# Optimization experiments

Measured on AMD Instinct MI355X. Metric: run time of the kernel, lower is better.

Reference implementation:

```python
import jax, jax.numpy as jnp
import numpy as np


def setup_inputs() -> dict:
    key = jax.random.key(0)
    k1, k2, k3 = jax.random.split(key, 3)
    B, F, D = 1024, 784, 512
    x = jax.random.normal(k1, (B, F), dtype=jnp.float32)
    # keras 'uniform' initializer ~ U(-0.05, 0.05)
    Wmin = jax.random.uniform(k2, (D, F), dtype=jnp.float32, minval=-0.05, maxval=0.05)
    Wmax = jax.random.uniform(k3, (D, F), dtype=jnp.float32, minval=-0.05, maxval=0.05)
    return {"x": x, "Wmin": Wmin, "Wmax": Wmax}


def reference(x, Wmin, Wmax):
    # x: [B, F]; Wmin, Wmax: [D, F]
    # L1[b,d] = min_f (x[b,f] - Wmin[d,f]); L2[b,d] = min_f (Wmax[d,f] - x[b,f])
    L1 = jnp.min(x[:, None, :] - Wmin[None, :, :], axis=2)  # [B, D]
    L2 = jnp.min(Wmax[None, :, :] - x[:, None, :], axis=2)  # [B, D]
    # activation is None (linear) in this config
    return jnp.minimum(L1, L2)  # [B, D]
```

## Files before the change

kernel.cpp:

```cpp
#include <hip/hip_runtime.h>


constexpr int F_DIM = 784;
constexpr int BK = 8;
constexpr int NCHUNK = F_DIM / BK;
constexpr int BM = 32;
constexpr int BN = 128;
constexpr int LSTR = BK + 4;
constexpr int ZSPLIT = 16;

typedef float f4v __attribute__((ext_vector_type(4)));
typedef float f2v __attribute__((ext_vector_type(2)));

__global__ __launch_bounds__(64, 3)
void dendral_main(const float* __restrict__ x,
                  const float* __restrict__ wmin,
                  const float* __restrict__ wmax,
                  float* __restrict__ dst,
                  int D, long long sliceN, int zsplit) {
  __shared__ float lx[BM * LSTR];
  __shared__ float lwn[BN * LSTR];
  __shared__ float lwx[BN * LSTR];

  const int l  = threadIdx.x;
  const int tx = l & 15;
  const int ty = l >> 4;
  const int b0 = blockIdx.x * BM;
  const int d0 = blockIdx.y * BN;
  const int z  = blockIdx.z;
  const int c0 = (z * NCHUNK) / zsplit;
  const int c1 = ((z + 1) * NCHUNK) / zsplit;

  const int sr = l >> 1;
  const int sc = (l & 1) << 2;
  const float* xg = x + (size_t)(b0 + sr) * F_DIM + sc;
  const float* ng = wmin + (size_t)(d0 + sr) * F_DIM + sc;
  const float* wg = wmax + (size_t)(d0 + sr) * F_DIM + sc;
  float* lds_x = lx + sr * LSTR + sc;
  float* lds_n = lwn + sr * LSTR + sc;
  float* lds_w = lwx + sr * LSTR + sc;
  const size_t wrow_step = (size_t)32 * F_DIM;
  const int    lrow_step = 32 * LSTR;

  float acc[8][8];
#pragma unroll
  for (int r = 0; r < 8; ++r)
#pragma unroll
    for (int c = 0; c < 8; ++c) acc[r][c] = __builtin_inff();

  for (int kc = c0; kc < c1; ++kc) {
    const int fo = kc * BK;
    f4v gx = *(const f4v*)(xg + fo);
    f4v gn[4], gw[4];
#pragma unroll
    for (int i = 0; i < 4; ++i) {
      gn[i] = *(const f4v*)(ng + i * wrow_step + fo);
      gw[i] = *(const f4v*)(wg + i * wrow_step + fo);
    }
    __syncthreads();
    *(f4v*)lds_x = gx;
#pragma unroll
    for (int i = 0; i < 4; ++i) {
      *(f4v*)(lds_n + i * lrow_step) = gn[i];
      *(f4v*)(lds_w + i * lrow_step) = gw[i];
    }
    __syncthreads();

#pragma unroll
    for (int f = 0; f < BK; f += 4) {
      f4v nv[8], wv[8];
#pragma unroll
      for (int c = 0; c < 8; ++c) {
        nv[c] = *(const f4v*)&lwn[(tx + 16 * c) * LSTR + f];
        wv[c] = *(const f4v*)&lwx[(tx + 16 * c) * LSTR + f];
      }
#pragma unroll
      for (int r = 0; r < 8; ++r) {
        f4v xv = *(const f4v*)&lx[(ty + 4 * r) * LSTR + f];
#pragma unroll
        for (int c = 0; c < 8; ++c) {
          f2v a_lo = xv.xy - nv[c].xy;
          f2v a_hi = xv.zw - nv[c].zw;
          f2v b_lo = wv[c].xy - xv.xy;
          f2v b_hi = wv[c].zw - xv.zw;
          float m = acc[r][c];
          m = fminf(m, fminf(a_lo.x, a_lo.y));
          m = fminf(m, fminf(a_hi.x, a_hi.y));
          m = fminf(m, fminf(b_lo.x, b_lo.y));
          m = fminf(m, fminf(b_hi.x, b_hi.y));
          acc[r][c] = m;
        }
      }
    }
  }

  float* o = dst + (size_t)z * sliceN;
#pragma unroll
  for (int r = 0; r < 8; ++r)
#pragma unroll
    for (int c = 0; c < 8; ++c) {
      const int b = b0 + ty + 4 * r;
      const int d = d0 + tx + 16 * c;
      o[(size_t)b * D + d] = acc[r][c];
    }
}

__global__ __launch_bounds__(256, 4)
void dendral_reduce(const float* __restrict__ ws, float* __restrict__ out,
                    long long sliceN, int zsplit) {
  const long long i = (long long)blockIdx.x * 256 + threadIdx.x;
  f4v m = ((const f4v*)ws)[i];
  for (int z = 1; z < zsplit; ++z) {
    f4v v = ((const f4v*)(ws + (size_t)z * sliceN))[i];
    m.x = fminf(m.x, v.x); m.y = fminf(m.y, v.y);
    m.z = fminf(m.z, v.z); m.w = fminf(m.w, v.w);
  }
  ((f4v*)out)[i] = m;
}

extern "C" void kernel_launch(void* const* d_in, const int* in_sizes, int n_in,
                              void* d_out, int out_size, void* d_ws, size_t ws_size,
                              hipStream_t stream) {
  const float* x    = (const float*)d_in[0];
  const float* wmin = (const float*)d_in[1];
  const float* wmax = (const float*)d_in[2];
  float* out = (float*)d_out;
  const int B = in_sizes[0] / F_DIM;
  const int D = in_sizes[1] / F_DIM;
  const long long sliceN = (long long)B * D;

  const int zsplit = (ws_size >= (size_t)ZSPLIT * sliceN * sizeof(float))
                         ? ZSPLIT : 1;
  float* dst = (zsplit > 1) ? (float*)d_ws : out;

  dim3 grid(B / BM, D / BN, zsplit);
  dendral_main<<<grid, 64, 0, stream>>>(x, wmin, wmax, dst, D, sliceN, zsplit);

  if (zsplit > 1) {
    dendral_reduce<<<(int)(sliceN / (256 * 4)), 256, 0, stream>>>(
        (const float*)d_ws, out, sliceN, zsplit);
  }
  (void)n_in; (void)out_size;
}
```

Baseline: 102.6 us.

## Prefetch next chunk into registers, force packed subtracts, reorder LDS reads

The global loads for the next K-chunk are now issued before the compute of the current chunk, so memory latency overlaps with the min-reduction math (register double buffering). The subtracts are forced into v_pk_add_f32 with negation via inline asm, and the inner loop now caches the 8 x vectors and streams the weight vectors per column. The occupancy hint drops from 3 to 2 waves per SIMD to make room for the extra prefetch registers, which reduces latency hiding from concurrent waves.

New measurement: 132.0 us. 28.6% more time.

```diff
diff --git a/kernel.cpp b/kernel.cpp
--- a/kernel.cpp
+++ b/kernel.cpp
@@ -12,7 +12,14 @@
 typedef float f4v __attribute__((ext_vector_type(4)));
 typedef float f2v __attribute__((ext_vector_type(2)));
 
-__global__ __launch_bounds__(64, 3)
+__device__ inline f2v pk_sub(f2v a, f2v b) {
+  f2v d;
+  asm("v_pk_add_f32 %0, %1, %2 neg_lo:[0,1] neg_hi:[0,1]"
+      : "=v"(d) : "v"(a), "v"(b));
+  return d;
+}
+
+__global__ __launch_bounds__(64, 2)
 void dendral_main(const float* __restrict__ x,
                   const float* __restrict__ wmin,
                   const float* __restrict__ wmax,
@@ -48,15 +55,15 @@
 #pragma unroll
     for (int c = 0; c < 8; ++c) acc[r][c] = __builtin_inff();
 
+  f4v gx = *(const f4v*)(xg + c0 * BK);
+  f4v gn[4], gw[4];
+#pragma unroll
+  for (int i = 0; i < 4; ++i) {
+    gn[i] = *(const f4v*)(ng + i * wrow_step + c0 * BK);
+    gw[i] = *(const f4v*)(wg + i * wrow_step + c0 * BK);
+  }
+
   for (int kc = c0; kc < c1; ++kc) {
-    const int fo = kc * BK;
-    f4v gx = *(const f4v*)(xg + fo);
-    f4v gn[4], gw[4];
-#pragma unroll
-    for (int i = 0; i < 4; ++i) {
-      gn[i] = *(const f4v*)(ng + i * wrow_step + fo);
-      gw[i] = *(const f4v*)(wg + i * wrow_step + fo);
-    }
     __syncthreads();
     *(f4v*)lds_x = gx;
 #pragma unroll
@@ -64,25 +71,33 @@
       *(f4v*)(lds_n + i * lrow_step) = gn[i];
       *(f4v*)(lds_w + i * lrow_step) = gw[i];
     }
+    if (kc + 1 < c1) {
+      const int fo = (kc + 1) * BK;
+      gx = *(const f4v*)(xg + fo);
+#pragma unroll
+      for (int i = 0; i < 4; ++i) {
+        gn[i] = *(const f4v*)(ng + i * wrow_step + fo);
+        gw[i] = *(const f4v*)(wg + i * wrow_step + fo);
+      }
+    }
     __syncthreads();
 
 #pragma unroll
     for (int f = 0; f < BK; f += 4) {
-      f4v nv[8], wv[8];
+      f4v xv[8];
+#pragma unroll
+      for (int r = 0; r < 8; ++r)
+        xv[r] = *(const f4v*)&lx[(ty + 4 * r) * LSTR + f];
 #pragma unroll
       for (int c = 0; c < 8; ++c) {
-        nv[c] = *(const f4v*)&lwn[(tx + 16 * c) * LSTR + f];
-        wv[c] = *(const f4v*)&lwx[(tx + 16 * c) * LSTR + f];
-      }
+        f4v nv = *(const f4v*)&lwn[(tx + 16 * c) * LSTR + f];
+        f4v wv = *(const f4v*)&lwx[(tx + 16 * c) * LSTR + f];
 #pragma unroll
-      for (int r = 0; r < 8; ++r) {
-        f4v xv = *(const f4v*)&lx[(ty + 4 * r) * LSTR + f];
-#pragma unroll
-        for (int c = 0; c < 8; ++c) {
-          f2v a_lo = xv.xy - nv[c].xy;
-          f2v a_hi = xv.zw - nv[c].zw;
-          f2v b_lo = wv[c].xy - xv.xy;
-          f2v b_hi = wv[c].zw - xv.zw;
+        for (int r = 0; r < 8; ++r) {
+          f2v a_lo = pk_sub(xv[r].xy, nv.xy);
+          f2v a_hi = pk_sub(xv[r].zw, nv.zw);
+          f2v b_lo = pk_sub(wv.xy, xv[r].xy);
+          f2v b_hi = pk_sub(wv.zw, xv[r].zw);
           float m = acc[r][c];
           m = fminf(m, fminf(a_lo.x, a_lo.y));
           m = fminf(m, fminf(a_hi.x, a_hi.y));
```
